# Kernel tuning notes

Hardware: AMD Instinct MI355X
Metric: run time of the kernel (lower is better)

The kernel has to match this reference:

```python
import jax, jax.numpy as jnp
import numpy as np

N_EMBD = 2048
N_HEAD = 16
HEAD_DIM = N_EMBD // N_HEAD
ROPE_THETA = 10000.0


def _rope_cache(seq_len, head_dim, theta):
    inv_freq = 1.0 / theta ** (jnp.arange(0, head_dim, 2, dtype=jnp.float32) / head_dim)
    t = jnp.arange(seq_len, dtype=jnp.float32)
    freqs = jnp.outer(t, inv_freq)  # [S, head_dim//2]
    return jnp.cos(freqs), jnp.sin(freqs)


def _apply_rope(x, cos, sin):
    # x: [B, H, S, D]; cos/sin: [S, D//2] -> broadcast over B, H
    cos = cos[None, None, :, :]
    sin = sin[None, None, :, :]
    x1 = x[..., ::2]
    x2 = x[..., 1::2]
    rot = jnp.stack((x1 * cos - x2 * sin, x1 * sin + x2 * cos), axis=-1)
    return rot.reshape(x.shape)


def setup_inputs() -> dict:
    key = jax.random.key(0)
    ks = jax.random.split(key, 5)
    scale = 1.0 / np.sqrt(N_EMBD)
    x = jax.random.normal(ks[0], (2, 2048, N_EMBD), dtype=jnp.float32)
    wq = jax.random.normal(ks[1], (N_EMBD, N_EMBD), dtype=jnp.float32) * scale
    wk = jax.random.normal(ks[2], (N_EMBD, N_EMBD), dtype=jnp.float32) * scale
    wv = jax.random.normal(ks[3], (N_EMBD, N_EMBD), dtype=jnp.float32) * scale
    wo = jax.random.normal(ks[4], (N_EMBD, N_EMBD), dtype=jnp.float32) * scale
    return {"x": x, "wq": wq, "wk": wk, "wv": wv, "wo": wo}


def reference(x, wq, wk, wv, wo):
    bsz, seq_len, _ = x.shape
    q = (x @ wq).reshape(bsz, seq_len, N_HEAD, HEAD_DIM).transpose(0, 2, 1, 3)
    k = (x @ wk).reshape(bsz, seq_len, N_HEAD, HEAD_DIM).transpose(0, 2, 1, 3)
    v = (x @ wv).reshape(bsz, seq_len, N_HEAD, HEAD_DIM).transpose(0, 2, 1, 3)

    cos, sin = _rope_cache(seq_len, HEAD_DIM, ROPE_THETA)
    q = _apply_rope(q, cos, sin)
    k = _apply_rope(k, cos, sin)

    scale = 1.0 / np.sqrt(HEAD_DIM)
    att = jnp.einsum('bhqd,bhkd->bhqk', q, k) * scale  # [B,H,S,S]
    causal = jnp.tril(jnp.ones((seq_len, seq_len), dtype=bool))
    att = jnp.where(causal[None, None, :, :], att, -jnp.inf)
    att = jax.nn.softmax(att, axis=-1)
    y = jnp.einsum('bhqk,bhkd->bhqd', att, v)  # [B,H,S,D]
    y = y.transpose(0, 2, 1, 3).reshape(bsz, seq_len, N_EMBD)
    return y @ wo
```

## Files before the change

### kernel.cpp

```cpp
#include <hip/hip_runtime.h>
#include <math.h>

constexpr int BSZ = 2;
constexpr int SEQ = 2048;
constexpr int NE  = 2048;
constexpr int NH  = 16;
constexpr int HD  = 128;
constexpr int MROWS = BSZ * SEQ;

typedef __bf16 bf16x8 __attribute__((ext_vector_type(8)));
typedef float  f32x4  __attribute__((ext_vector_type(4)));

__device__ __forceinline__ unsigned short f2bf(float f) {
    union { float f; unsigned u; } v; v.f = f;
    unsigned r = v.u + 0x7fffu + ((v.u >> 16) & 1u);
    return (unsigned short)(r >> 16);
}
__device__ __forceinline__ float bf2f(unsigned short s) {
    union { unsigned u; float f; } v; v.u = ((unsigned)s) << 16; return v.f;
}

__device__ __forceinline__ void load_lds16(const void* g, void* l) {
    __builtin_amdgcn_global_load_lds(
        (const __attribute__((address_space(1))) unsigned int*)g,
        (__attribute__((address_space(3))) unsigned int*)l, 16, 0, 0);
}

template <int CTRL>
__device__ __forceinline__ float dpp_mv(float x) {
    int v = __builtin_amdgcn_update_dpp(
        0, __builtin_bit_cast(int, x), CTRL, 0xF, 0xF, true);
    return __builtin_bit_cast(float, v);
}
__device__ __forceinline__ float row16_max(float x) {
    x = fmaxf(x, dpp_mv<0xB1>(x));
    x = fmaxf(x, dpp_mv<0x4E>(x));
    x = fmaxf(x, dpp_mv<0x124>(x));
    x = fmaxf(x, dpp_mv<0x128>(x));
    return x;
}
__device__ __forceinline__ float row16_sum(float x) {
    x += dpp_mv<0xB1>(x);
    x += dpp_mv<0x4E>(x);
    x += dpp_mv<0x124>(x);
    x += dpp_mv<0x128>(x);
    return x;
}

__global__ __launch_bounds__(256) void transpose_cast(const float* __restrict__ xf,
                                                      const float* __restrict__ w0,
                                                      const float* __restrict__ w1,
                                                      const float* __restrict__ w2,
                                                      const float* __restrict__ w3,
                                                      ushort* __restrict__ xb,
                                                      ushort* __restrict__ o0,
                                                      ushort* __restrict__ o1,
                                                      ushort* __restrict__ o2,
                                                      ushort* __restrict__ o3)
{
    if (blockIdx.z == 4) {
        const int tid = threadIdx.y * 32 + threadIdx.x;
        const size_t i = (((size_t)blockIdx.y * 64 + blockIdx.x) * 256 + tid) * 8;
        float4 v0 = *(const float4*)(xf + i);
        float4 v1 = *(const float4*)(xf + i + 4);
        ushort4 a, b;
        a.x = f2bf(v0.x); a.y = f2bf(v0.y); a.z = f2bf(v0.z); a.w = f2bf(v0.w);
        b.x = f2bf(v1.x); b.y = f2bf(v1.y); b.z = f2bf(v1.z); b.w = f2bf(v1.w);
        *(ushort4*)(xb + i)     = a;
        *(ushort4*)(xb + i + 4) = b;
        return;
    }

    const float* S; ushort* D;
    switch (blockIdx.z) {
        case 0: S = w0; D = o0; break;
        case 1: S = w1; D = o1; break;
        case 2: S = w2; D = o2; break;
        default: S = w3; D = o3; break;
    }
    __shared__ float t[32][33];
    const int tx = threadIdx.x, ty = threadIdx.y;
    const int x0 = blockIdx.x * 32, y0 = blockIdx.y * 32;
#pragma unroll
    for (int i = 0; i < 4; ++i)
        t[ty + i * 8][tx] = S[(size_t)(y0 + ty + i * 8) * NE + x0 + tx];
    __syncthreads();
#pragma unroll
    for (int i = 0; i < 4; ++i)
        D[(size_t)(x0 + ty + i * 8) * NE + y0 + tx] = f2bf(t[tx][ty + i * 8]);
}

__global__ __launch_bounds__(256) void gemm_qkv(const ushort* __restrict__ A,
                                                const ushort* __restrict__ W,
                                                ushort* __restrict__ Qb,
                                                ushort* __restrict__ Kb,
                                                ushort* __restrict__ Vt)
{
    __shared__ ushort Al[128 * 64];
    __shared__ ushort Bl[128 * 64];

    const int tid  = threadIdx.x;
    const int w    = tid >> 6;
    const int lane = tid & 63;
    const int quad = lane >> 4;
    const int r    = lane & 15;
    const int wm   = w & 1;
    const int wn   = w >> 1;
    const int m0 = blockIdx.y * 128;
    const int n0 = blockIdx.x * 128;
    const int K  = NE;

    const int srow = tid >> 3;
    const int scol = ((tid & 7) ^ ((tid >> 3) & 7)) * 8;

    f32x4 acc[4][4] = {};

    for (int k0 = 0; k0 < K; k0 += 64) {
#pragma unroll
        for (int j = 0; j < 4; ++j) {
            load_lds16(A + (size_t)(m0 + j * 32 + srow) * K + k0 + scol,
                       &Al[j * 2048 + w * 512]);
            load_lds16(W + (size_t)(n0 + j * 32 + srow) * K + k0 + scol,
                       &Bl[j * 2048 + w * 512]);
        }
        __syncthreads();

#pragma unroll
        for (int kh = 0; kh < 2; ++kh) {
            const int sw = (((kh << 2) + quad) ^ (r & 7)) * 8;
            bf16x8 af[4], bfr[4];
#pragma unroll
            for (int it = 0; it < 4; ++it)
                af[it] = *(const bf16x8*)&Al[(wm * 64 + it * 16 + r) * 64 + sw];
#pragma unroll
            for (int jt = 0; jt < 4; ++jt)
                bfr[jt] = *(const bf16x8*)&Bl[(wn * 64 + jt * 16 + r) * 64 + sw];
#pragma unroll
            for (int it = 0; it < 4; ++it)
#pragma unroll
                for (int jt = 0; jt < 4; ++jt)
                    acc[it][jt] = __builtin_amdgcn_mfma_f32_16x16x32_bf16(
                        af[it], bfr[jt], acc[it][jt], 0, 0, 0);
        }
        __syncthreads();
    }

    const int mat  = n0 >> 11;
    const int ncol = n0 & 2047;
    if (mat < 2) {
        ushort* C = mat ? Kb : Qb;
        float invf[4];
#pragma unroll
        for (int jt = 0; jt < 4; ++jt) {
            const int d = (wn * 64 + jt * 16 + r) & 127;
            invf[jt] = exp2f((float)(d >> 1) * -0.20762050593046014f);
        }
        const float sgn = (r & 1) ? 1.0f : -1.0f;
#pragma unroll
        for (int it = 0; it < 4; ++it) {
            const int row = m0 + wm * 64 + it * 16 + quad * 4;
#pragma unroll
            for (int jt = 0; jt < 4; ++jt) {
                const int col = ncol + wn * 64 + jt * 16 + r;
#pragma unroll
                for (int reg = 0; reg < 4; ++reg) {
                    const float self = acc[it][jt][reg];
                    const float part = dpp_mv<0xB1>(self);
                    const int s = (row + reg) & 2047;
                    const float f = (float)s * invf[jt];
                    const float sn = __sinf(f);
                    const float cs = __cosf(f);
                    const float y = self * cs + sgn * part * sn;
                    C[(size_t)(row + reg) * NE + col] = f2bf(y);
                }
            }
        }
    } else {
#pragma unroll
        for (int it = 0; it < 4; ++it) {
            const int row = m0 + wm * 64 + it * 16 + quad * 4;
            const int bb = row >> 11;
            const int s  = row & 2047;
#pragma unroll
            for (int jt = 0; jt < 4; ++jt) {
                const int col = ncol + wn * 64 + jt * 16 + r;
                const int hh = col >> 7;
                const int d  = col & 127;
                ushort4 pk;
                pk.x = f2bf(acc[it][jt][0]); pk.y = f2bf(acc[it][jt][1]);
                pk.z = f2bf(acc[it][jt][2]); pk.w = f2bf(acc[it][jt][3]);
                *(ushort4*)&Vt[((size_t)((bb * NH + hh) * HD + d)) * SEQ + s] = pk;
            }
        }
    }
}

__global__ __launch_bounds__(256) void gemm_out(const ushort* __restrict__ A,
                                                const ushort* __restrict__ Bt,
                                                float* __restrict__ C)
{
    __shared__ ushort Al[128 * 64];
    __shared__ ushort Bl[128 * 64];

    const int tid  = threadIdx.x;
    const int w    = tid >> 6;
    const int lane = tid & 63;
    const int quad = lane >> 4;
    const int r    = lane & 15;
    const int wm   = w & 1;
    const int wn   = w >> 1;
    const int m0 = blockIdx.y * 128;
    const int n0 = blockIdx.x * 128;
    const int K  = NE;

    const int srow = tid >> 3;
    const int scol = ((tid & 7) ^ ((tid >> 3) & 7)) * 8;

    f32x4 acc[4][4] = {};

    for (int k0 = 0; k0 < K; k0 += 64) {
#pragma unroll
        for (int j = 0; j < 4; ++j) {
            load_lds16(A  + (size_t)(m0 + j * 32 + srow) * K + k0 + scol,
                       &Al[j * 2048 + w * 512]);
            load_lds16(Bt + (size_t)(n0 + j * 32 + srow) * K + k0 + scol,
                       &Bl[j * 2048 + w * 512]);
        }
        __syncthreads();

#pragma unroll
        for (int kh = 0; kh < 2; ++kh) {
            const int sw = (((kh << 2) + quad) ^ (r & 7)) * 8;
            bf16x8 af[4], bfr[4];
#pragma unroll
            for (int it = 0; it < 4; ++it)
                af[it] = *(const bf16x8*)&Al[(wm * 64 + it * 16 + r) * 64 + sw];
#pragma unroll
            for (int jt = 0; jt < 4; ++jt)
                bfr[jt] = *(const bf16x8*)&Bl[(wn * 64 + jt * 16 + r) * 64 + sw];
#pragma unroll
            for (int it = 0; it < 4; ++it)
#pragma unroll
                for (int jt = 0; jt < 4; ++jt)
                    acc[it][jt] = __builtin_amdgcn_mfma_f32_16x16x32_bf16(
                        af[it], bfr[jt], acc[it][jt], 0, 0, 0);
        }
        __syncthreads();
    }

#pragma unroll
    for (int it = 0; it < 4; ++it) {
        const int row = m0 + wm * 64 + it * 16 + quad * 4;
#pragma unroll
        for (int jt = 0; jt < 4; ++jt) {
            const int col = n0 + wn * 64 + jt * 16 + r;
#pragma unroll
            for (int reg = 0; reg < 4; ++reg)
                C[(size_t)(row + reg) * NE + col] = acc[it][jt][reg];
        }
    }
}

__global__ __launch_bounds__(256, 2) void flash_attn(const ushort* __restrict__ Qg,
                                                     const ushort* __restrict__ Kg,
                                                     const ushort* __restrict__ Vtg,
                                                     ushort* __restrict__ Yg)
{
    const int qt = (int)gridDim.x - 1 - (int)blockIdx.x;
    const int bh = blockIdx.y;
    const int b = bh >> 4, h = bh & 15;
    const int tid  = threadIdx.x;
    const int w    = tid >> 6;
    const int lane = tid & 63;
    const int quad = lane >> 4;
    const int r    = lane & 15;

    __shared__ ushort Ks[64][128];
    __shared__ ushort Vts[128][64];
    __shared__ ushort Ps[64][64];

    const int q0 = qt * 64;
    const size_t qkbase = (size_t)b * SEQ * NE + (size_t)h * HD;
    const size_t vbase  = (size_t)(bh * HD) * SEQ;
    const float scale = 0.088388347648318447f;

    bf16x8 aq[4];
    {
        const ushort* qrow = Qg + qkbase + (size_t)(q0 + w * 16 + r) * NE;
#pragma unroll
        for (int kc = 0; kc < 4; ++kc)
            aq[kc] = *(const bf16x8*)(qrow + kc * 32 + quad * 8);
    }

    float m_i[4], l_i[4];
    f32x4 acc_o[8];
#pragma unroll
    for (int reg = 0; reg < 4; ++reg) { m_i[reg] = -INFINITY; l_i[reg] = 0.f; }
#pragma unroll
    for (int dt = 0; dt < 8; ++dt) acc_o[dt] = f32x4{0.f, 0.f, 0.f, 0.f};

    const int rx = r & 7;

    for (int t = 0; t <= qt; ++t) {
        const int j0 = t * 64;

        {
            const int row0 = tid >> 4;
            const int ks   = tid & 15;
#pragma unroll
            for (int i = 0; i < 4; ++i) {
                const int row = i * 16 + row0;
                *(uint4*)&Ks[row][(ks ^ (row & 7)) * 8] =
                    *(const uint4*)(Kg + qkbase + (size_t)(j0 + row) * NE + ks * 8);
            }
            const int d0 = tid >> 3;
            const int vs = tid & 7;
#pragma unroll
            for (int i = 0; i < 4; ++i) {
                const int d = i * 32 + d0;
                *(uint4*)&Vts[d][(vs ^ (d & 7)) * 8] =
                    *(const uint4*)(Vtg + vbase + (size_t)d * SEQ + j0 + vs * 8);
            }
        }
        __syncthreads();

        __builtin_amdgcn_s_setprio(1);
        f32x4 sa[4];
#pragma unroll
        for (int jt = 0; jt < 4; ++jt) {
            f32x4 acc = {0.f, 0.f, 0.f, 0.f};
#pragma unroll
            for (int kc = 0; kc < 4; ++kc) {
                bf16x8 bk = *(const bf16x8*)&Ks[jt * 16 + r][((kc * 4 + quad) ^ rx) * 8];
                acc = __builtin_amdgcn_mfma_f32_16x16x32_bf16(aq[kc], bk, acc, 0, 0, 0);
            }
            sa[jt] = acc;
        }
        __builtin_amdgcn_s_setprio(0);

        if (t == qt) {
#pragma unroll
            for (int jt = 0; jt < 4; ++jt)
#pragma unroll
                for (int reg = 0; reg < 4; ++reg)
                    sa[jt][reg] = (jt * 16 + r > w * 16 + quad * 4 + reg)
                                  ? -INFINITY : sa[jt][reg] * scale;
        } else {
#pragma unroll
            for (int jt = 0; jt < 4; ++jt)
#pragma unroll
                for (int reg = 0; reg < 4; ++reg)
                    sa[jt][reg] *= scale;
        }

        float rmax[4], alpha[4], rsum[4];
#pragma unroll
        for (int reg = 0; reg < 4; ++reg) {
            rmax[reg] = fmaxf(fmaxf(sa[0][reg], sa[1][reg]),
                              fmaxf(sa[2][reg], sa[3][reg]));
            rmax[reg] = row16_max(rmax[reg]);
        }

#pragma unroll
        for (int reg = 0; reg < 4; ++reg) {
            const float mnew = fmaxf(m_i[reg], rmax[reg]);
            alpha[reg] = __expf(m_i[reg] - mnew);
            m_i[reg] = mnew;
            rsum[reg] = 0.f;
        }
#pragma unroll
        for (int jt = 0; jt < 4; ++jt)
#pragma unroll
            for (int reg = 0; reg < 4; ++reg) {
                const float p = __expf(sa[jt][reg] - m_i[reg]);
                sa[jt][reg] = p;
                rsum[reg] += p;
            }
#pragma unroll
        for (int reg = 0; reg < 4; ++reg) {
            rsum[reg] = row16_sum(rsum[reg]);
            l_i[reg] = l_i[reg] * alpha[reg] + rsum[reg];
        }

#pragma unroll
        for (int jt = 0; jt < 4; ++jt)
#pragma unroll
            for (int reg = 0; reg < 4; ++reg) {
                const int prow = w * 16 + quad * 4 + reg;
                const int pcol = jt * 16 + r;
                Ps[prow][((((pcol >> 3) ^ (prow & 7)) << 3) | (pcol & 7))]
                    = f2bf(sa[jt][reg]);
            }

#pragma unroll
        for (int dt = 0; dt < 8; ++dt)
#pragma unroll
            for (int reg = 0; reg < 4; ++reg)
                acc_o[dt][reg] *= alpha[reg];

        bf16x8 ap[2];
#pragma unroll
        for (int kc = 0; kc < 2; ++kc)
            ap[kc] = *(const bf16x8*)&Ps[w * 16 + r][((kc * 4 + quad) ^ rx) * 8];
        __builtin_amdgcn_s_setprio(1);
#pragma unroll
        for (int dt = 0; dt < 8; ++dt)
#pragma unroll
            for (int kc = 0; kc < 2; ++kc) {
                bf16x8 bv = *(const bf16x8*)&Vts[dt * 16 + r][((kc * 4 + quad) ^ rx) * 8];
                acc_o[dt] = __builtin_amdgcn_mfma_f32_16x16x32_bf16(ap[kc], bv, acc_o[dt], 0, 0, 0);
            }
        __builtin_amdgcn_s_setprio(0);
        __syncthreads();
    }

#pragma unroll
    for (int reg = 0; reg < 4; ++reg) {
        const float inv = 1.0f / l_i[reg];
        const size_t rowbase = qkbase + (size_t)(q0 + w * 16 + quad * 4 + reg) * NE;
#pragma unroll
        for (int dt = 0; dt < 8; ++dt)
            Yg[rowbase + dt * 16 + r] = f2bf(acc_o[dt][reg] * inv);
    }
}

extern "C" void kernel_launch(void* const* d_in, const int* in_sizes, int n_in,
                              void* d_out, int out_size, void* d_ws, size_t ws_size,
                              hipStream_t stream)
{
    const float* x  = (const float*)d_in[0];
    const float* wq = (const float*)d_in[1];
    const float* wk = (const float*)d_in[2];
    const float* wv = (const float*)d_in[3];
    const float* wo = (const float*)d_in[4];
    float* out = (float*)d_out;

    ushort* ws = (ushort*)d_ws;
    const size_t MAT  = (size_t)MROWS * NE;
    const size_t WMAT = (size_t)NE * NE;
    ushort* xb  = ws;
    ushort* wqT = xb + MAT;
    ushort* wkT = wqT + WMAT;
    ushort* wvT = wkT + WMAT;
    ushort* woT = wvT + WMAT;
    ushort* Qb  = woT + WMAT;
    ushort* Kb  = Qb + MAT;
    ushort* Vt  = Kb + MAT;
    ushort* Yb  = Qb;

    transpose_cast<<<dim3(64, 64, 5), dim3(32, 8), 0, stream>>>(
        x, wq, wk, wv, wo, xb, wqT, wkT, wvT, woT);

    gemm_qkv<<<dim3(48, 32), 256, 0, stream>>>(xb, wqT, Qb, Kb, Vt);

    flash_attn<<<dim3(SEQ / 64, BSZ * NH), 256, 0, stream>>>(Qb, Kb, Vt, Yb);

    gemm_out<<<dim3(16, 32), 256, 0, stream>>>(Yb, woT, out);
}
```

Before: 428.9 us.

## Use direct global-to-LDS loads for K/V and lazy softmax rescaling

K and V tile loads into LDS now use global_load_lds, so data no longer passes through registers, with the XOR swizzle moved into the global source address. The online softmax also rescales the output accumulators and running sum only when some row's max grows by more than a threshold (wave-uniform check), which skips most exp and multiply work per tile. The risk is a larger exp range in fp32 and bf16 P values exceeding 1, plus correctness depending on the per-lane LDS address layout matching the swizzle.

Measured after the change: 435.0 us. Within noise of the previous version (+1.4%).

```diff
diff --git a/kernel.cpp b/kernel.cpp
--- a/kernel.cpp
+++ b/kernel.cpp
@@ -300,27 +300,27 @@
     for (int dt = 0; dt < 8; ++dt) acc_o[dt] = f32x4{0.f, 0.f, 0.f, 0.f};
 
     const int rx = r & 7;
+    const int kl4 = lane >> 4;
+    const int kl15 = lane & 15;
+    const int vl3 = lane >> 3;
+    const int vl7 = lane & 7;
 
     for (int t = 0; t <= qt; ++t) {
         const int j0 = t * 64;
 
-        {
-            const int row0 = tid >> 4;
-            const int ks   = tid & 15;
-#pragma unroll
-            for (int i = 0; i < 4; ++i) {
-                const int row = i * 16 + row0;
-                *(uint4*)&Ks[row][(ks ^ (row & 7)) * 8] =
-                    *(const uint4*)(Kg + qkbase + (size_t)(j0 + row) * NE + ks * 8);
-            }
-            const int d0 = tid >> 3;
-            const int vs = tid & 7;
-#pragma unroll
-            for (int i = 0; i < 4; ++i) {
-                const int d = i * 32 + d0;
-                *(uint4*)&Vts[d][(vs ^ (d & 7)) * 8] =
-                    *(const uint4*)(Vtg + vbase + (size_t)d * SEQ + j0 + vs * 8);
-            }
+#pragma unroll
+        for (int i = 0; i < 4; ++i) {
+            const int row = i * 16 + w * 4 + kl4;
+            const int sc  = (kl15 ^ (row & 7)) * 8;
+            load_lds16(Kg + qkbase + (size_t)(j0 + row) * NE + sc,
+                       &Ks[i * 16 + w * 4][0]);
+        }
+#pragma unroll
+        for (int i = 0; i < 4; ++i) {
+            const int d  = i * 32 + w * 8 + vl3;
+            const int sc = (vl7 ^ (d & 7)) * 8;
+            load_lds16(Vtg + vbase + (size_t)d * SEQ + j0 + sc,
+                       &Vts[i * 32 + w * 8][0]);
         }
         __syncthreads();
 
@@ -353,7 +353,7 @@
                     sa[jt][reg] *= scale;
         }
 
-        float rmax[4], alpha[4], rsum[4];
+        float rmax[4], rsum[4];
 #pragma unroll
         for (int reg = 0; reg < 4; ++reg) {
             rmax[reg] = fmaxf(fmaxf(sa[0][reg], sa[1][reg]),
@@ -361,13 +361,30 @@
             rmax[reg] = row16_max(rmax[reg]);
         }
 
-#pragma unroll
-        for (int reg = 0; reg < 4; ++reg) {
-            const float mnew = fmaxf(m_i[reg], rmax[reg]);
-            alpha[reg] = __expf(m_i[reg] - mnew);
-            m_i[reg] = mnew;
-            rsum[reg] = 0.f;
-        }
+        bool grow = false;
+#pragma unroll
+        for (int reg = 0; reg < 4; ++reg)
+            grow = grow || (rmax[reg] > m_i[reg] + 8.0f);
+        if (__any(grow)) {
+            float alpha[4];
+#pragma unroll
+            for (int reg = 0; reg < 4; ++reg) {
+                const float mnew = fmaxf(m_i[reg], rmax[reg]);
+                alpha[reg] = __expf(m_i[reg] - mnew);
+                m_i[reg] = mnew;
+            }
+#pragma unroll
+            for (int dt = 0; dt < 8; ++dt)
+#pragma unroll
+                for (int reg = 0; reg < 4; ++reg)
+                    acc_o[dt][reg] *= alpha[reg];
+#pragma unroll
+            for (int reg = 0; reg < 4; ++reg)
+                l_i[reg] *= alpha[reg];
+        }
+
+#pragma unroll
+        for (int reg = 0; reg < 4; ++reg) rsum[reg] = 0.f;
 #pragma unroll
         for (int jt = 0; jt < 4; ++jt)
 #pragma unroll
@@ -379,7 +396,7 @@
 #pragma unroll
         for (int reg = 0; reg < 4; ++reg) {
             rsum[reg] = row16_sum(rsum[reg]);
-            l_i[reg] = l_i[reg] * alpha[reg] + rsum[reg];
+            l_i[reg] += rsum[reg];
         }
 
 #pragma unroll
@@ -391,12 +408,6 @@
                 Ps[prow][((((pcol >> 3) ^ (prow & 7)) << 3) | (pcol & 7))]
                     = f2bf(sa[jt][reg]);
             }
-
-#pragma unroll
-        for (int dt = 0; dt < 8; ++dt)
-#pragma unroll
-            for (int reg = 0; reg < 4; ++reg)
-                acc_o[dt][reg] *= alpha[reg];
 
         bf16x8 ap[2];
 #pragma unroll
```
